# Optimization experiments

Hardware: AMD Instinct MI355X
Metric: run time of the kernel (lower is better)

The kernel has to match this reference:

```python
import jax, jax.numpy as jnp
import numpy as np

EPS = 1e-6

def _ste(x, xq):
    return x + jax.lax.stop_gradient(xq - x)

def rmsnorm(x, w):
    return x * jax.lax.rsqrt(jnp.mean(x * x, axis=-1, keepdims=True) + EPS) * w

def act_quant(x):
    # per-token absmax int8 quantization (BitNet b1.58)
    s = 127.0 / jnp.clip(jnp.max(jnp.abs(x), axis=-1, keepdims=True), 1e-5)
    return _ste(x, jnp.clip(jnp.round(x * s), -128, 127) / s)

def w_quant(w):
    # per-tensor mean-absmax ternary quantization
    s = 1.0 / jnp.clip(jnp.mean(jnp.abs(w)), 1e-5)
    return _ste(w, jnp.clip(jnp.round(w * s), -1, 1) / s)

def bitlinear(x, w):
    return act_quant(x) @ w_quant(w).T

def snake_beta(x, log_a, log_b):
    a = jnp.exp(log_a)
    b = jnp.exp(log_b)
    s = jnp.sin(a * x)
    return x + (1.0 / (b + 1e-9)) * s * s

def ffn(x, nw, w1, la, lb, w2):
    h = bitlinear(rmsnorm(x, nw), w1)
    return bitlinear(snake_beta(h, la, lb), w2)

def mha(x, nw, ipw, ipb, opw, opb, num_heads):
    B, T, D = x.shape
    hd = D // num_heads
    xn = rmsnorm(x, nw)
    qkv = xn @ ipw.T + ipb  # [B,T,3D]
    q, k, v = jnp.split(qkv, 3, axis=-1)
    def heads(t):
        return t.reshape(B, T, num_heads, hd).transpose(0, 2, 1, 3)  # [B,H,T,hd]
    q, k, v = heads(q), heads(k), heads(v)
    scores = jnp.einsum('bhqd,bhkd->bhqk', q, k) / jnp.sqrt(jnp.asarray(hd, x.dtype))
    attn = jax.nn.softmax(scores, axis=-1)
    o = jnp.einsum('bhqk,bhkd->bhqd', attn, v)
    o = o.transpose(0, 2, 1, 3).reshape(B, T, D)
    return o @ opw.T + opb

def conv_branch(x, nw, pw1, dw, dwb, bg, bb, bm, bv, la, lb, pw2, K):
    B, T, D = x.shape
    h = rmsnorm(x, nw)
    h = bitlinear(h, pw1)  # [B,T,2D] (1x1 BitConv1d)
    a, g = jnp.split(h, 2, axis=-1)
    h = a * jax.nn.sigmoid(g)  # GLU over channels
    hc = h.transpose(0, 2, 1)  # [B,D,T]
    hc = jax.lax.conv_general_dilated(
        hc, dw, window_strides=(1,), padding=[(K // 2, K // 2)],
        feature_group_count=D, dimension_numbers=('NCH', 'OIH', 'NCH'))
    hc = hc + dwb[None, :, None]
    hc = (hc - bm[None, :, None]) * jax.lax.rsqrt(bv[None, :, None] + 1e-5) * bg[None, :, None] + bb[None, :, None]
    h = hc.transpose(0, 2, 1)  # [B,T,D]
    h = snake_beta(h, la, lb)
    return bitlinear(h, pw2)

def setup_inputs() -> dict:
    key = jax.random.key(0)
    B, T, D, H, K = 4, 2048, 512, 8, 31
    ks = jax.random.split(key, 16)
    n = lambda k, s: (jax.random.normal(k, s, jnp.float32) * 0.02)
    d = {
        'x': jax.random.normal(ks[0], (B, T, D), jnp.float32),
        'ff1_norm_w': jnp.ones((D,), jnp.float32),
        'ff1_w1': n(ks[1], (4 * D, D)), 'ff1_a': jnp.zeros((4 * D,), jnp.float32),
        'ff1_b': jnp.zeros((4 * D,), jnp.float32), 'ff1_w2': n(ks[2], (D, 4 * D)),
        'attn_norm_w': jnp.ones((D,), jnp.float32),
        'in_proj_w': n(ks[3], (3 * D, D)), 'in_proj_b': jnp.zeros((3 * D,), jnp.float32),
        'out_proj_w': n(ks[4], (D, D)), 'out_proj_b': jnp.zeros((D,), jnp.float32),
        'conv_norm_w': jnp.ones((D,), jnp.float32),
        'pw1_w': n(ks[5], (2 * D, D)),
        'dw_w': n(ks[6], (D, 1, K)), 'dw_b': jnp.zeros((D,), jnp.float32),
        'bn_g': jnp.ones((D,), jnp.float32), 'bn_b': jnp.zeros((D,), jnp.float32),
        'bn_m': jnp.zeros((D,), jnp.float32), 'bn_v': jnp.ones((D,), jnp.float32),
        'snake_a': jnp.zeros((D,), jnp.float32), 'snake_b': jnp.zeros((D,), jnp.float32),
        'pw2_w': n(ks[7], (D, D)),
        'ff2_norm_w': jnp.ones((D,), jnp.float32),
        'ff2_w1': n(ks[8], (4 * D, D)), 'ff2_a': jnp.zeros((4 * D,), jnp.float32),
        'ff2_b': jnp.zeros((4 * D,), jnp.float32), 'ff2_w2': n(ks[9], (D, 4 * D)),
        'final_norm_w': jnp.ones((D,), jnp.float32),
    }
    return d

def reference(x, ff1_norm_w, ff1_w1, ff1_a, ff1_b, ff1_w2, attn_norm_w, in_proj_w, in_proj_b, out_proj_w, out_proj_b, conv_norm_w, pw1_w, dw_w, dw_b, bn_g, bn_b, bn_m, bn_v, snake_a, snake_b, pw2_w, ff2_norm_w, ff2_w1, ff2_a, ff2_b, ff2_w2, final_norm_w):
    H, K = 8, 31
    x = x + 0.5 * ffn(x, ff1_norm_w, ff1_w1, ff1_a, ff1_b, ff1_w2)
    x = x + mha(x, attn_norm_w, in_proj_w, in_proj_b, out_proj_w, out_proj_b, H)
    x = x + conv_branch(x, conv_norm_w, pw1_w, dw_w, dw_b, bn_g, bn_b, bn_m, bn_v, snake_a, snake_b, pw2_w, K)
    x = x + 0.5 * ffn(x, ff2_norm_w, ff2_w1, ff2_a, ff2_b, ff2_w2)
    return rmsnorm(x, final_norm_w)
```

## Files before the change

### kernel.cpp

```cpp
#include <hip/hip_runtime.h>
#include <math.h>


typedef int   v4i __attribute__((ext_vector_type(4)));
typedef float v4f __attribute__((ext_vector_type(4)));
typedef float v16f __attribute__((ext_vector_type(16)));
typedef short v8s __attribute__((ext_vector_type(8)));
typedef unsigned short u16;

#define GLOAD_LDS(g, l) __builtin_amdgcn_global_load_lds( \
    (const __attribute__((address_space(1))) void*)(g),   \
    (__attribute__((address_space(3))) void*)(l), 16, 0, 0)

__device__ __forceinline__ float blk_sum256(float v, float* sm) {
#pragma unroll
  for (int m = 32; m; m >>= 1) v += __shfl_xor(v, m);
  int w = threadIdx.x >> 6;
  __syncthreads();
  if ((threadIdx.x & 63) == 0) sm[w] = v;
  __syncthreads();
  return sm[0] + sm[1] + sm[2] + sm[3];
}

__device__ __forceinline__ u16 f2bf(float f) {
  union { float f; unsigned u; } x;
  x.f = f;
  unsigned r = x.u + 0x7fffu + ((x.u >> 16) & 1u);
  return (u16)(r >> 16);
}

__device__ __forceinline__ float bf2f(u16 u) {
  union { unsigned u; float f; } x;
  x.u = ((unsigned)u) << 16;
  return x.f;
}

__device__ __forceinline__ void xcd_tiles(int& tx, int& ty) {
  int nx = gridDim.x;
  int flat = blockIdx.y * nx + blockIdx.x;
  int nwg = nx * gridDim.y;
  int cpx = nwg >> 3;
  int swz = (flat & 7) * cpx + (flat >> 3);
  ty = swz / nx;
  tx = swz - ty * nx;
}

__global__ __launch_bounds__(256) void wabs_stage1(
    const float* __restrict__ w0, const float* __restrict__ w1,
    const float* __restrict__ w2, const float* __restrict__ w3,
    const float* __restrict__ w4, const float* __restrict__ w5,
    float* __restrict__ part) {
  __shared__ float sm[4];
  const float* ws[6] = {w0, w1, w2, w3, w4, w5};
  const int ns[6] = {1048576, 1048576, 524288, 262144, 1048576, 1048576};
  int widx = blockIdx.x >> 6;
  int chunk = blockIdx.x & 63;
  const float* w = ws[widx];
  int n = ns[widx];
  float s = 0.f;
  for (int i = chunk * 256 + threadIdx.x; i < n; i += 64 * 256) s += fabsf(w[i]);
  s = blk_sum256(s, sm);
  if (threadIdx.x == 0) part[widx * 64 + chunk] = s;
}

__global__ __launch_bounds__(256) void wquant_all(
    const float* __restrict__ w0, const float* __restrict__ w1,
    const float* __restrict__ w2, const float* __restrict__ w3,
    const float* __restrict__ w4, const float* __restrict__ w5,
    const float* __restrict__ part, float* __restrict__ scales,
    signed char* __restrict__ out) {
  const float* ws[6] = {w0, w1, w2, w3, w4, w5};
  const int ns[6] = {1048576, 1048576, 524288, 262144, 1048576, 1048576};
  const int offs[6] = {0, 1048576, 2097152, 2621440, 2883584, 3932160};
  int widx = blockIdx.y;
  const float* w = ws[widx];
  int n = ns[widx];
  signed char* o = out + offs[widx];
  float ssum = 0.f;
#pragma unroll 8
  for (int i = 0; i < 64; ++i) ssum += part[widx * 64 + i];
  float wsc = fmaxf(ssum / (float)n, 1e-5f);
  if (blockIdx.x == 0 && threadIdx.x == 0) scales[widx] = wsc;
  float s = 1.0f / wsc;
  for (int i = blockIdx.x * 256 + threadIdx.x; i < n; i += 128 * 256)
    o[i] = (signed char)(int)fminf(fmaxf(rintf(w[i] * s), -1.f), 1.f);
}

__global__ __launch_bounds__(256) void wcvt_tabs(
    const float* __restrict__ ip, const float* __restrict__ op, u16* __restrict__ wb,
    const float* __restrict__ a1, const float* __restrict__ b1,
    const float* __restrict__ a2, const float* __restrict__ b2,
    float* __restrict__ tabs) {
  int bid = blockIdx.x;
  if (bid < 1024) {
    int i = bid * 256 + threadIdx.x;
    float4 f;
    if (i < 196608) f = *(const float4*)(ip + (size_t)i * 4);
    else f = *(const float4*)(op + (size_t)(i - 196608) * 4);
    u16* dst = wb + (size_t)i * 4;
    dst[0] = f2bf(f.x); dst[1] = f2bf(f.y); dst[2] = f2bf(f.z); dst[3] = f2bf(f.w);
  } else {
    int i = (bid - 1024) * 256 + threadIdx.x;
    if (i < 2048) {
      tabs[i] = __expf(a1[i]);
      tabs[2048 + i] = 1.0f / (__expf(b1[i]) + 1e-9f);
      tabs[4096 + i] = __expf(a2[i]);
      tabs[6144 + i] = 1.0f / (__expf(b2[i]) + 1e-9f);
    }
  }
}

__global__ __launch_bounds__(256) void rmsnorm_f32x(
    const float* __restrict__ x, const float* __restrict__ w,
    signed char* __restrict__ out8, u16* __restrict__ xbf,
    float* __restrict__ dq) {
  const int tid = threadIdx.x;
  const int lane = tid & 63, wv = tid >> 6;
  const int row = blockIdx.x * 4 + wv;
  const int c0 = lane * 8;
  const float* xr = x + (size_t)row * 512 + c0;
  float4 f0 = *(const float4*)xr;
  float4 f1 = *(const float4*)(xr + 4);
  float fin[8] = {f0.x, f0.y, f0.z, f0.w, f1.x, f1.y, f1.z, f1.w};
  v8s xb;
  float v[8];
  float ss = 0.f;
#pragma unroll
  for (int j = 0; j < 8; ++j) {
    u16 b = f2bf(fin[j]);
    xb[j] = (short)b;
    v[j] = bf2f(b);
    ss = fmaf(v[j], v[j], ss);
  }
  *(v8s*)(xbf + (size_t)row * 512 + c0) = xb;
#pragma unroll
  for (int m = 1; m < 64; m <<= 1) ss += __shfl_xor(ss, m);
  float sc = 1.0f / sqrtf(ss * (1.0f / 512.0f) + 1e-6f);
  float4 w0 = *(const float4*)(w + c0);
  float4 w1 = *(const float4*)(w + c0 + 4);
  float wv8[8] = {w0.x, w0.y, w0.z, w0.w, w1.x, w1.y, w1.z, w1.w};
  float y[8];
  float am = 0.f;
#pragma unroll
  for (int j = 0; j < 8; ++j) {
    y[j] = v[j] * sc * wv8[j];
    am = fmaxf(am, fabsf(y[j]));
  }
#pragma unroll
  for (int m = 1; m < 64; m <<= 1) am = fmaxf(am, __shfl_xor(am, m));
  float amc = fmaxf(am, 1e-5f);
  float s = 127.0f / amc;
  unsigned long long pkt = 0;
#pragma unroll
  for (int j = 0; j < 8; ++j) {
    int q = (int)rintf(y[j] * s);
    pkt |= ((unsigned long long)(unsigned char)(signed char)q) << (8 * j);
  }
  *(unsigned long long*)(out8 + (size_t)row * 512 + c0) = pkt;
  if (lane == 0) dq[row] = amc * (1.0f / 127.0f);
}

__global__ __launch_bounds__(256) void rmsnorm_wave(
    const u16* __restrict__ x, const float* __restrict__ w, int mode,
    float* __restrict__ outf, signed char* __restrict__ out8,
    u16* __restrict__ outb, float* __restrict__ dq) {
  const int tid = threadIdx.x;
  const int lane = tid & 63, wv = tid >> 6;
  const int row = blockIdx.x * 4 + wv;
  const int c0 = lane * 8;
  v8s xv = *(const v8s*)(x + (size_t)row * 512 + c0);
  float v[8];
  float ss = 0.f;
#pragma unroll
  for (int j = 0; j < 8; ++j) {
    v[j] = bf2f((u16)xv[j]);
    ss = fmaf(v[j], v[j], ss);
  }
#pragma unroll
  for (int m = 1; m < 64; m <<= 1) ss += __shfl_xor(ss, m);
  float sc = 1.0f / sqrtf(ss * (1.0f / 512.0f) + 1e-6f);
  float4 w0 = *(const float4*)(w + c0);
  float4 w1 = *(const float4*)(w + c0 + 4);
  float wv8[8] = {w0.x, w0.y, w0.z, w0.w, w1.x, w1.y, w1.z, w1.w};
  float y[8];
#pragma unroll
  for (int j = 0; j < 8; ++j) y[j] = v[j] * sc * wv8[j];
  if (mode == 0) {
    float* o = outf + (size_t)row * 512 + c0;
    *(float4*)o = make_float4(y[0], y[1], y[2], y[3]);
    *(float4*)(o + 4) = make_float4(y[4], y[5], y[6], y[7]);
  } else if (mode == 1) {
    float am = 0.f;
#pragma unroll
    for (int j = 0; j < 8; ++j) am = fmaxf(am, fabsf(y[j]));
#pragma unroll
    for (int m = 1; m < 64; m <<= 1) am = fmaxf(am, __shfl_xor(am, m));
    float amc = fmaxf(am, 1e-5f);
    float s = 127.0f / amc;
    unsigned long long pkt = 0;
#pragma unroll
    for (int j = 0; j < 8; ++j) {
      int q = (int)rintf(y[j] * s);
      pkt |= ((unsigned long long)(unsigned char)(signed char)q) << (8 * j);
    }
    *(unsigned long long*)(out8 + (size_t)row * 512 + c0) = pkt;
    if (lane == 0) dq[row] = amc * (1.0f / 127.0f);
  } else {
    v8s o;
#pragma unroll
    for (int j = 0; j < 8; ++j) o[j] = (short)f2bf(y[j]);
    *(v8s*)(outb + (size_t)row * 512 + c0) = o;
  }
}

__global__ __launch_bounds__(256) void snake_wave(
    const u16* __restrict__ h, const float* __restrict__ ta, const float* __restrict__ tb,
    signed char* __restrict__ out, float* __restrict__ dq) {
  const int tid = threadIdx.x;
  const int lane = tid & 63, wv = tid >> 6;
  const int row = blockIdx.x * 4 + wv;
  const u16* hr = h + (size_t)row * 2048;
  float vals[32];
  float am = 0.f;
#pragma unroll
  for (int g = 0; g < 4; ++g) {
    int c0 = g * 512 + lane * 8;
    v8s hv = *(const v8s*)(hr + c0);
    float4 ta0 = *(const float4*)(ta + c0);
    float4 ta1 = *(const float4*)(ta + c0 + 4);
    float4 tb0 = *(const float4*)(tb + c0);
    float4 tb1 = *(const float4*)(tb + c0 + 4);
    float sa[8] = {ta0.x, ta0.y, ta0.z, ta0.w, ta1.x, ta1.y, ta1.z, ta1.w};
    float sib[8] = {tb0.x, tb0.y, tb0.z, tb0.w, tb1.x, tb1.y, tb1.z, tb1.w};
#pragma unroll
    for (int j = 0; j < 8; ++j) {
      float v = bf2f((u16)hv[j]);
      float s = __sinf(sa[j] * v);
      v += s * s * sib[j];
      vals[g * 8 + j] = v;
      am = fmaxf(am, fabsf(v));
    }
  }
#pragma unroll
  for (int m = 1; m < 64; m <<= 1) am = fmaxf(am, __shfl_xor(am, m));
  float amc = fmaxf(am, 1e-5f);
  float s = 127.0f / amc;
#pragma unroll
  for (int g = 0; g < 4; ++g) {
    unsigned long long pkt = 0;
#pragma unroll
    for (int j = 0; j < 8; ++j) {
      int q = (int)rintf(vals[g * 8 + j] * s);
      pkt |= ((unsigned long long)(unsigned char)(signed char)q) << (8 * j);
    }
    *(unsigned long long*)(out + (size_t)row * 2048 + g * 512 + lane * 8) = pkt;
  }
  if (lane == 0) dq[row] = amc * (1.0f / 127.0f);
}

__global__ __launch_bounds__(256) void rowquant_wave(
    const u16* __restrict__ in, signed char* __restrict__ out, float* __restrict__ dq) {
  const int tid = threadIdx.x;
  const int lane = tid & 63, wv = tid >> 6;
  const int row = blockIdx.x * 4 + wv;
  const int c0 = lane * 8;
  v8s xv = *(const v8s*)(in + (size_t)row * 512 + c0);
  float v[8];
  float am = 0.f;
#pragma unroll
  for (int j = 0; j < 8; ++j) {
    v[j] = bf2f((u16)xv[j]);
    am = fmaxf(am, fabsf(v[j]));
  }
#pragma unroll
  for (int m = 1; m < 64; m <<= 1) am = fmaxf(am, __shfl_xor(am, m));
  float amc = fmaxf(am, 1e-5f);
  float s = 127.0f / amc;
  unsigned long long pkt = 0;
#pragma unroll
  for (int j = 0; j < 8; ++j) {
    int q = (int)rintf(v[j] * s);
    pkt |= ((unsigned long long)(unsigned char)(signed char)q) << (8 * j);
  }
  *(unsigned long long*)(out + (size_t)row * 512 + c0) = pkt;
  if (lane == 0) dq[row] = amc * (1.0f / 127.0f);
}

template <int BN, int OM>
__global__ __launch_bounds__(256) void gemm_i8_t(
    const signed char* __restrict__ A, const signed char* __restrict__ B,
    const float* __restrict__ wsp, const float* __restrict__ adq,
    const u16* __restrict__ resid, float rscale,
    u16* __restrict__ outb, int N, int K) {
  constexpr int JF = BN / 32;
  __shared__ signed char As[16384];
  __shared__ signed char Bs[BN * 128];
  const int tid = threadIdx.x;
  int txc, tyc;
  xcd_tiles(txc, tyc);
  const int m0 = tyc << 7;
  const int n0 = txc * BN;
  const int lane = tid & 63;
  const int wv = tid >> 6;
  const int wr = (wv >> 1) << 6, wc = (wv & 1) * (16 * JF);
  const int r15 = lane & 15, khi = lane >> 4;
  const int srow = tid >> 3;
  const int sslot = (tid & 7) ^ (srow & 7);
  const signed char* Ag = A + (size_t)(m0 + srow) * K + sslot * 16;
  const signed char* Bg = B + (size_t)(n0 + srow) * K + sslot * 16;
  const size_t row32 = (size_t)32 * K;

  int aoff[4][2], boff[JF][2];
#pragma unroll
  for (int i = 0; i < 4; ++i) {
    int r = wr + i * 16 + r15;
#pragma unroll
    for (int s = 0; s < 2; ++s)
      aoff[i][s] = r * 128 + (((s << 2) + khi) ^ (r & 7)) * 16;
  }
#pragma unroll
  for (int j = 0; j < JF; ++j) {
    int c = wc + j * 16 + r15;
#pragma unroll
    for (int s = 0; s < 2; ++s)
      boff[j][s] = c * 128 + (((s << 2) + khi) ^ (c & 7)) * 16;
  }
  v4i acc[4][JF] = {};
  for (int k0 = 0; k0 < K; k0 += 128) {
    __syncthreads();
#pragma unroll
    for (int c = 0; c < 4; ++c)
      GLOAD_LDS(Ag + c * row32 + k0, As + c * 4096 + tid * 16);
#pragma unroll
    for (int c = 0; c < BN / 32; ++c)
      GLOAD_LDS(Bg + c * row32 + k0, Bs + c * 4096 + tid * 16);
    __syncthreads();
    v4i a[4][2], b[JF][2];
#pragma unroll
    for (int i = 0; i < 4; ++i) {
      a[i][0] = *(const v4i*)(As + aoff[i][0]);
      a[i][1] = *(const v4i*)(As + aoff[i][1]);
    }
#pragma unroll
    for (int j = 0; j < JF; ++j) {
      b[j][0] = *(const v4i*)(Bs + boff[j][0]);
      b[j][1] = *(const v4i*)(Bs + boff[j][1]);
    }
#pragma unroll
    for (int i = 0; i < 4; ++i)
#pragma unroll
      for (int j = 0; j < JF; ++j) {
        acc[i][j] = __builtin_amdgcn_mfma_i32_16x16x64_i8(a[i][0], b[j][0], acc[i][j], 0, 0, 0);
        acc[i][j] = __builtin_amdgcn_mfma_i32_16x16x64_i8(a[i][1], b[j][1], acc[i][j], 0, 0, 0);
      }
  }
  const float wsc = *wsp;
#pragma unroll
  for (int i = 0; i < 4; ++i) {
    int rb = m0 + wr + i * 16 + (khi << 2);
    float dqv[4];
#pragma unroll
    for (int rr = 0; rr < 4; ++rr) dqv[rr] = adq[rb + rr] * wsc;
#pragma unroll
    for (int j = 0; j < JF; ++j) {
      int col = n0 + wc + j * 16 + r15;
#pragma unroll
      for (int rr = 0; rr < 4; ++rr) {
        size_t idx = (size_t)(rb + rr) * N + col;
        float v = (float)acc[i][j][rr] * dqv[rr];
        if constexpr (OM == 0) outb[idx] = f2bf(v);
        else outb[idx] = f2bf(fmaf(rscale, v, bf2f(resid[idx])));
      }
    }
  }
}

template <int BN, int OM>
__global__ __launch_bounds__(256) void gemm_bf16_t(
    const u16* __restrict__ A, const u16* __restrict__ B,
    const float* __restrict__ bias, const u16* __restrict__ resid,
    u16* __restrict__ outb, int N, int K) {
  constexpr int JF = BN / 32;
  __shared__ signed char As[8192];
  __shared__ signed char Bs[BN * 64];
  const int tid = threadIdx.x;
  int txc, tyc;
  xcd_tiles(txc, tyc);
  const int m0 = tyc << 7;
  const int n0 = txc * BN;
  const int lane = tid & 63;
  const int wv = tid >> 6;
  const int wr = (wv >> 1) << 6, wc = (wv & 1) * (16 * JF);
  const int r15 = lane & 15, khi = lane >> 4;
  const int srow = tid >> 2;
  const int sslot = (tid & 3) ^ ((srow >> 1) & 3);
  const int K2 = K * 2;
  const signed char* Ag = (const signed char*)A + (size_t)(m0 + srow) * K2 + sslot * 16;
  const signed char* Bg = (const signed char*)B + (size_t)(n0 + srow) * K2 + sslot * 16;
  const size_t half = (size_t)64 * K2;

  int aoff[4], boff[JF];
#pragma unroll
  for (int i = 0; i < 4; ++i) {
    int r = wr + i * 16 + r15;
    aoff[i] = r * 64 + ((khi ^ ((r >> 1) & 3)) << 4);
  }
#pragma unroll
  for (int j = 0; j < JF; ++j) {
    int c = wc + j * 16 + r15;
    boff[j] = c * 64 + ((khi ^ ((c >> 1) & 3)) << 4);
  }
  v4f acc[4][JF] = {};
  for (int kb = 0; kb < K2; kb += 64) {
    __syncthreads();
    GLOAD_LDS(Ag + kb, As + tid * 16);
    GLOAD_LDS(Ag + half + kb, As + 4096 + tid * 16);
    GLOAD_LDS(Bg + kb, Bs + tid * 16);
    if constexpr (BN == 128) GLOAD_LDS(Bg + half + kb, Bs + 4096 + tid * 16);
    __syncthreads();
    v8s a[4], b[JF];
#pragma unroll
    for (int i = 0; i < 4; ++i) a[i] = *(const v8s*)(As + aoff[i]);
#pragma unroll
    for (int j = 0; j < JF; ++j) b[j] = *(const v8s*)(Bs + boff[j]);
#pragma unroll
    for (int i = 0; i < 4; ++i)
#pragma unroll
      for (int j = 0; j < JF; ++j)
        acc[i][j] = __builtin_amdgcn_mfma_f32_16x16x32_bf16(a[i], b[j], acc[i][j], 0, 0, 0);
  }
#pragma unroll
  for (int i = 0; i < 4; ++i) {
    int rb = m0 + wr + i * 16 + (khi << 2);
#pragma unroll
    for (int j = 0; j < JF; ++j) {
      int col = n0 + wc + j * 16 + r15;
      float bv = bias[col];
#pragma unroll
      for (int rr = 0; rr < 4; ++rr) {
        float v = acc[i][j][rr] + bv;
        if constexpr (OM == 2) {
          int rowb = rb + rr;
          int tin = rowb & 31;
          int seg = col >> 9;
          int cc = col & 511;
          int h2 = cc >> 6, d = cc & 63;
          size_t base = ((size_t)(((rowb >> 11) * 8 + h2) * 64 + ((rowb & 2047) >> 5))) * 6144;
          size_t off;
          if (seg == 0)
            off = (size_t)(8 + (d >> 4)) * 512 + ((((d >> 3) & 1) << 5) + tin) * 8 + (d & 7);
          else if (seg == 1)
            off = (size_t)(d >> 4) * 512 + ((((d >> 3) & 1) << 5) + tin) * 8 + (d & 7);
          else
            off = (size_t)(4 + ((d >> 5) << 1) + (tin >> 4)) * 512 +
                  ((((tin >> 3) & 1) << 5) + (d & 31)) * 8 + (tin & 7);
          outb[base + off] = f2bf(v);
        } else {
          size_t idx = (size_t)(rb + rr) * N + col;
          if constexpr (OM == 0) outb[idx] = f2bf(v);
          else outb[idx] = f2bf(bf2f(resid[idx]) + v);
        }
      }
    }
  }
}

__global__ __launch_bounds__(256) void attn32(
    const u16* __restrict__ kvqp, u16* __restrict__ opart, float* __restrict__ ml) {
  __shared__ u16 KV[2][4096];
  const int tid = threadIdx.x;
  const int lane = tid & 63;
  const int wv = tid >> 6;
  const int l31 = lane & 31;
  const int hi = lane >> 5;
  const int bh = blockIdx.y;
  const int z = blockIdx.z;
  const int b = bh >> 3, h = bh & 7;
  const int qt = blockIdx.x * 4 + wv;
  const int q0 = qt << 5;
  const float C = 0.18033688011112042f;

  v8s qf[4];
  {
    const u16* qb = kvqp + ((size_t)(bh * 64 + qt)) * 6144 + lane * 8;
#pragma unroll
    for (int ks = 0; ks < 4; ++ks) qf[ks] = *(const v8s*)(qb + (8 + ks) * 512);
  }
  v16f o0 = {}, o1 = {};
  float l_run = 0.f;

  const u16* tb = kvqp + ((size_t)(bh * 64 + z * 32)) * 6144;

  GLOAD_LDS(tb + tid * 8, &KV[0][tid * 8]);
  GLOAD_LDS(tb + 2048 + tid * 8, &KV[0][2048 + tid * 8]);
  __syncthreads();

  int cur = 0;
  for (int t = 0; t < 32; ++t) {
    if (t < 31) {
      const u16* nb = tb + (size_t)(t + 1) * 6144;
      GLOAD_LDS(nb + tid * 8, &KV[cur ^ 1][tid * 8]);
      GLOAD_LDS(nb + 2048 + tid * 8, &KV[cur ^ 1][2048 + tid * 8]);
    }
    v8s kf[4], vf[4];
#pragma unroll
    for (int ks = 0; ks < 4; ++ks) kf[ks] = *(const v8s*)(&KV[cur][ks * 512 + lane * 8]);
#pragma unroll
    for (int j = 0; j < 4; ++j) vf[j] = *(const v8s*)(&KV[cur][2048 + j * 512 + lane * 8]);

    __builtin_amdgcn_s_setprio(1);
    v16f sacc = {};
#pragma unroll
    for (int ks = 0; ks < 4; ++ks)
      sacc = __builtin_amdgcn_mfma_f32_32x32x16_bf16(kf[ks], qf[ks], sacc, 0, 0, 0);
    __builtin_amdgcn_s_setprio(0);

    float s[16];
#pragma unroll
    for (int r = 0; r < 16; ++r) s[r] = exp2f(sacc[r] * C);

    {
      float a0 = (s[0] + s[1]) + (s[2] + s[3]);
      float a1 = (s[4] + s[5]) + (s[6] + s[7]);
      float a2 = (s[8] + s[9]) + (s[10] + s[11]);
      float a3 = (s[12] + s[13]) + (s[14] + s[15]);
      float ls = (a0 + a1) + (a2 + a3);
      float tsw = ls;
      asm("v_permlane32_swap_b32 %0, %1" : "+v"(tsw), "+v"(ls));
      l_run += ls + tsw;
    }

    unsigned pk[8];
#pragma unroll
    for (int g = 0; g < 8; ++g) {
      unsigned u;
      asm("v_cvt_pk_bf16_f32 %0, %1, %2" : "=v"(u) : "v"(s[2 * g]), "v"(s[2 * g + 1]));
      pk[g] = u;
    }
    asm("v_permlane32_swap_b32 %0, %1" : "+v"(pk[2]), "+v"(pk[0]));
    asm("v_permlane32_swap_b32 %0, %1" : "+v"(pk[3]), "+v"(pk[1]));
    asm("v_permlane32_swap_b32 %0, %1" : "+v"(pk[6]), "+v"(pk[4]));
    asm("v_permlane32_swap_b32 %0, %1" : "+v"(pk[7]), "+v"(pk[5]));
    v4i w0, w1;
    w0[0] = pk[0]; w0[1] = pk[1]; w0[2] = pk[2]; w0[3] = pk[3];
    w1[0] = pk[4]; w1[1] = pk[5]; w1[2] = pk[6]; w1[3] = pk[7];
    v8s pf0 = *(v8s*)&w0;
    v8s pf1 = *(v8s*)&w1;

    __builtin_amdgcn_s_setprio(1);
    o0 = __builtin_amdgcn_mfma_f32_32x32x16_bf16(vf[0], pf0, o0, 0, 0, 0);
    o0 = __builtin_amdgcn_mfma_f32_32x32x16_bf16(vf[1], pf1, o0, 0, 0, 0);
    o1 = __builtin_amdgcn_mfma_f32_32x32x16_bf16(vf[2], pf0, o1, 0, 0, 0);
    o1 = __builtin_amdgcn_mfma_f32_32x32x16_bf16(vf[3], pf1, o1, 0, 0, 0);
    __builtin_amdgcn_s_setprio(0);

    __syncthreads();
    cur ^= 1;
  }

  float inv = 1.0f / l_run;
  u16* orow = opart + (size_t)z * 4194304 + (size_t)(b * 2048 + q0 + l31) * 512 + h * 64;
#pragma unroll
  for (int dt = 0; dt < 2; ++dt) {
#pragma unroll
    for (int g = 0; g < 8; ++g) {
      int d = dt * 32 + ((2 * g) & 3) + 8 * (g >> 1) + 4 * hi;
      float a = (dt ? o1[2 * g] : o0[2 * g]) * inv;
      float bv = (dt ? o1[2 * g + 1] : o0[2 * g + 1]) * inv;
      unsigned u;
      asm("v_cvt_pk_bf16_f32 %0, %1, %2" : "=v"(u) : "v"(a), "v"(bv));
      *(unsigned*)(orow + d) = u;
    }
  }
  if (hi == 0) {
    size_t mi = (size_t)(z * 8192 + b * 2048 + q0 + l31) * 8 + h;
    ml[mi] = l_run;
  }
}

__global__ __launch_bounds__(256) void attn_merge(
    const u16* __restrict__ opart, const float* __restrict__ ml,
    u16* __restrict__ attno) {
  __shared__ float wsm[2][8];
  const int r = blockIdx.x, tid = threadIdx.x;
  if (tid < 8) {
    float l0 = ml[(size_t)r * 8 + tid];
    float l1 = ml[(size_t)(8192 + r) * 8 + tid];
    float inv = 1.0f / (l0 + l1);
    wsm[0][tid] = l0 * inv;
    wsm[1][tid] = l1 * inv;
  }
  __syncthreads();
  int c = tid * 2;
  int hh = c >> 6;
  float x0 = 0.f, x1 = 0.f;
#pragma unroll
  for (int z = 0; z < 2; ++z) {
    unsigned p = *(const unsigned*)(opart + (size_t)z * 4194304 + (size_t)r * 512 + c);
    float w = wsm[z][hh];
    x0 = fmaf(bf2f((u16)p), w, x0);
    x1 = fmaf(bf2f((u16)(p >> 16)), w, x1);
  }
  unsigned u;
  asm("v_cvt_pk_bf16_f32 %0, %1, %2" : "=v"(u) : "v"(x0), "v"(x1));
  *(unsigned*)(attno + (size_t)r * 512 + c) = u;
}

__global__ __launch_bounds__(256) void dwconv_fused(
    const u16* __restrict__ g3, const float* __restrict__ dww,
    const float* __restrict__ dwb, const float* __restrict__ bng,
    const float* __restrict__ bnb, const float* __restrict__ bnm,
    const float* __restrict__ bnv, const float* __restrict__ la,
    const float* __restrict__ lb, u16* __restrict__ outp) {
  __shared__ float IN[160 * 64];
  __shared__ float WT[1984];
  __shared__ float PRM[4][64];
  const int tid = threadIdx.x;
  const int cg = blockIdx.x << 6;
  const int t0 = blockIdx.y << 7;
  const int bb = blockIdx.z;

  if (tid < 64) {
    int c = cg + tid;
    float sc = bng[c] / sqrtf(bnv[c] + 1e-5f);
    PRM[0][tid] = sc;
    PRM[1][tid] = (dwb[c] - bnm[c]) * sc + bnb[c];
    PRM[2][tid] = __expf(la[c]);
    PRM[3][tid] = 1.0f / (__expf(lb[c]) + 1e-9f);
  }
  for (int i = tid; i < 1984; i += 256) WT[i] = dww[cg * 31 + i];

#pragma unroll
  for (int p = 0; p < 5; ++p) {
    int r = p * 32 + (tid >> 3);
    int t = t0 - 16 + r;
    int c8 = (tid & 7) << 3;
    float4 lo = make_float4(0.f, 0.f, 0.f, 0.f);
    float4 hv = make_float4(0.f, 0.f, 0.f, 0.f);
    if (t >= 0 && t < 2048) {
      const u16* rp = g3 + ((size_t)(bb * 2048 + t)) * 1024 + cg + c8;
      v8s a8 = *(const v8s*)rp;
      v8s g8 = *(const v8s*)(rp + 512);
      float va[8];
#pragma unroll
      for (int j = 0; j < 8; ++j) {
        float fa = bf2f((u16)a8[j]);
        float fg = bf2f((u16)g8[j]);
        va[j] = fa / (1.f + __expf(-fg));
      }
      lo = make_float4(va[0], va[1], va[2], va[3]);
      hv = make_float4(va[4], va[5], va[6], va[7]);
    }
    *(float4*)&IN[r * 64 + c8] = lo;
    *(float4*)&IN[r * 64 + c8 + 4] = hv;
  }
  __syncthreads();

  const int ch = tid & 63;
  const int tg = tid >> 6;
  const float sc = PRM[0][ch], sh = PRM[1][ch], sa = PRM[2][ch], sib = PRM[3][ch];
  float w[31];
#pragma unroll
  for (int k = 0; k < 31; ++k) w[k] = WT[ch * 31 + k];

  for (int pass = 0; pass < 4; ++pass) {
    int tl = pass * 32 + tg * 8;
    float x[38];
#pragma unroll
    for (int i = 0; i < 38; ++i) x[i] = IN[(tl + 1 + i) * 64 + ch];
    float acc[8] = {0.f, 0.f, 0.f, 0.f, 0.f, 0.f, 0.f, 0.f};
#pragma unroll
    for (int k = 0; k < 31; ++k)
#pragma unroll
      for (int j = 0; j < 8; ++j) acc[j] = fmaf(x[k + j], w[k], acc[j]);
#pragma unroll
    for (int j = 0; j < 8; ++j) {
      float v = acc[j] * sc + sh;
      float s = __sinf(sa * v);
      v += s * s * sib;
      outp[((size_t)(bb * 2048 + t0 + tl + j)) * 512 + cg + ch] = f2bf(v);
    }
  }
}

extern "C" void kernel_launch(void* const* d_in, const int* in_sizes, int n_in,
                              void* d_out, int out_size, void* d_ws, size_t ws_size,
                              hipStream_t stream) {
  const float* x_in = (const float*)d_in[0];
  const float* ff1_norm_w = (const float*)d_in[1];
  const float* ff1_w1 = (const float*)d_in[2];
  const float* ff1_a = (const float*)d_in[3];
  const float* ff1_b = (const float*)d_in[4];
  const float* ff1_w2 = (const float*)d_in[5];
  const float* attn_norm_w = (const float*)d_in[6];
  const float* in_proj_w = (const float*)d_in[7];
  const float* in_proj_b = (const float*)d_in[8];
  const float* out_proj_w = (const float*)d_in[9];
  const float* out_proj_b = (const float*)d_in[10];
  const float* conv_norm_w = (const float*)d_in[11];
  const float* pw1_w = (const float*)d_in[12];
  const float* dw_w = (const float*)d_in[13];
  const float* dw_b = (const float*)d_in[14];
  const float* bn_g = (const float*)d_in[15];
  const float* bn_b = (const float*)d_in[16];
  const float* bn_m = (const float*)d_in[17];
  const float* bn_v = (const float*)d_in[18];
  const float* snake_a = (const float*)d_in[19];
  const float* snake_b = (const float*)d_in[20];
  const float* pw2_w = (const float*)d_in[21];
  const float* ff2_norm_w = (const float*)d_in[22];
  const float* ff2_w1 = (const float*)d_in[23];
  const float* ff2_a = (const float*)d_in[24];
  const float* ff2_b = (const float*)d_in[25];
  const float* ff2_w2 = (const float*)d_in[26];
  const float* final_norm_w = (const float*)d_in[27];
  float* out = (float*)d_out;

  char* ws = (char*)d_ws;
  u16* x_bf = (u16*)(ws + 0);
  u16* x_cur = (u16*)(ws + 8388608);
  u16* kvqp = (u16*)(ws + 41943040);
  u16* opart = (u16*)(ws + 67108864);
  u16* attno = (u16*)(ws + 100663296);
  float* ml = (float*)(ws + 109051904);
  u16* h_b = (u16*)(ws + 16777216);
  u16* g3b = (u16*)(ws + 16777216);
  u16* convout = (u16*)(ws + 50331648);
  signed char* a8a = (signed char*)(ws + 83886080);
  signed char* a8b = (signed char*)(ws + 88080384);
  u16* xnb = (u16*)(ws + 104857600);
  signed char* wq = (signed char*)(ws + 113246208);
  signed char* wq_w1 = wq;
  signed char* wq_w2 = wq + 1048576;
  signed char* wq_p1 = wq + 2097152;
  signed char* wq_p2 = wq + 2621440;
  signed char* wq_f21 = wq + 2883584;
  signed char* wq_f22 = wq + 3932160;
  u16* wb = (u16*)(ws + 118226944);
  u16* wb_ip = wb;
  u16* wb_op = wb + 786432;
  float* scales = (float*)(ws + 120324096);
  float* partials = (float*)(ws + 120324352);
  float* ascale = (float*)(ws + 120325888);
  float* tabs = (float*)(ws + 120358912);

  wabs_stage1<<<384, 256, 0, stream>>>(ff1_w1, ff1_w2, pw1_w, pw2_w, ff2_w1, ff2_w2, partials);
  wquant_all<<<dim3(128, 6), 256, 0, stream>>>(ff1_w1, ff1_w2, pw1_w, pw2_w, ff2_w1, ff2_w2,
                                               partials, scales, wq);
  wcvt_tabs<<<1032, 256, 0, stream>>>(in_proj_w, out_proj_w, wb, ff1_a, ff1_b, ff2_a, ff2_b,
                                      tabs);

  rmsnorm_f32x<<<2048, 256, 0, stream>>>(x_in, ff1_norm_w, a8a, x_bf, ascale);
  gemm_i8_t<128, 0><<<dim3(16, 64), 256, 0, stream>>>(
      a8a, wq_w1, scales + 0, ascale, nullptr, 1.0f, h_b, 2048, 512);
  snake_wave<<<2048, 256, 0, stream>>>(h_b, tabs, tabs + 2048, a8b, ascale);
  gemm_i8_t<64, 1><<<dim3(8, 64), 256, 0, stream>>>(
      a8b, wq_w2, scales + 1, ascale, x_bf, 0.5f, x_cur, 512, 2048);

  rmsnorm_wave<<<2048, 256, 0, stream>>>(x_cur, attn_norm_w, 2, nullptr, nullptr, xnb, nullptr);
  gemm_bf16_t<128, 2><<<dim3(12, 64), 256, 0, stream>>>(
      xnb, wb_ip, in_proj_b, nullptr, kvqp, 1536, 512);
  attn32<<<dim3(16, 32, 2), 256, 0, stream>>>(kvqp, opart, ml);
  attn_merge<<<8192, 256, 0, stream>>>(opart, ml, attno);
  gemm_bf16_t<64, 1><<<dim3(8, 64), 256, 0, stream>>>(
      attno, wb_op, out_proj_b, x_cur, x_cur, 512, 512);

  rmsnorm_wave<<<2048, 256, 0, stream>>>(x_cur, conv_norm_w, 1, nullptr, a8a, nullptr, ascale);
  gemm_i8_t<128, 0><<<dim3(8, 64), 256, 0, stream>>>(
      a8a, wq_p1, scales + 2, ascale, nullptr, 1.0f, g3b, 1024, 512);
  dwconv_fused<<<dim3(8, 16, 4), 256, 0, stream>>>(g3b, dw_w, dw_b, bn_g, bn_b, bn_m, bn_v,
                                                   snake_a, snake_b, convout);
  rowquant_wave<<<2048, 256, 0, stream>>>(convout, a8a, ascale);
  gemm_i8_t<64, 1><<<dim3(8, 64), 256, 0, stream>>>(
      a8a, wq_p2, scales + 3, ascale, x_cur, 1.0f, x_cur, 512, 512);

  rmsnorm_wave<<<2048, 256, 0, stream>>>(x_cur, ff2_norm_w, 1, nullptr, a8a, nullptr, ascale);
  gemm_i8_t<128, 0><<<dim3(16, 64), 256, 0, stream>>>(
      a8a, wq_f21, scales + 4, ascale, nullptr, 1.0f, h_b, 2048, 512);
  snake_wave<<<2048, 256, 0, stream>>>(h_b, tabs + 4096, tabs + 6144, a8b, ascale);
  gemm_i8_t<64, 1><<<dim3(8, 64), 256, 0, stream>>>(
      a8b, wq_f22, scales + 5, ascale, x_cur, 0.5f, x_cur, 512, 2048);

  rmsnorm_wave<<<2048, 256, 0, stream>>>(x_cur, final_norm_w, 0, out, nullptr, nullptr, nullptr);
}
```

Baseline: 297.9 us.

## Fuse snake activation into FFN1 GEMM epilogue and drop attention split-K merge

The snake-beta activation moves into the epilogue of the first FFN int8 GEMM, using a new OM==2 mode, so the following row-quant kernel only computes absmax and quantizes. Separately, attention no longer splits the key range in two along blockIdx.z. Each block now loops over all 64 key tiles and writes the normalized output directly, which removes the partial-output buffer writes and the attn_merge kernel. In exchange the attention grid is halved, so there is less parallelism and a longer serial loop per block. The sin in the epilogue also adds some work to the GEMM.

```diff
diff --git a/kernel.cpp b/kernel.cpp
--- a/kernel.cpp
+++ b/kernel.cpp
@@ -213,9 +213,8 @@
   }
 }
 
-__global__ __launch_bounds__(256) void snake_wave(
-    const u16* __restrict__ h, const float* __restrict__ ta, const float* __restrict__ tb,
-    signed char* __restrict__ out, float* __restrict__ dq) {
+__global__ __launch_bounds__(256) void rq2048_wave(
+    const u16* __restrict__ h, signed char* __restrict__ out, float* __restrict__ dq) {
   const int tid = threadIdx.x;
   const int lane = tid & 63, wv = tid >> 6;
   const int row = blockIdx.x * 4 + wv;
@@ -226,17 +225,9 @@
   for (int g = 0; g < 4; ++g) {
     int c0 = g * 512 + lane * 8;
     v8s hv = *(const v8s*)(hr + c0);
-    float4 ta0 = *(const float4*)(ta + c0);
-    float4 ta1 = *(const float4*)(ta + c0 + 4);
-    float4 tb0 = *(const float4*)(tb + c0);
-    float4 tb1 = *(const float4*)(tb + c0 + 4);
-    float sa[8] = {ta0.x, ta0.y, ta0.z, ta0.w, ta1.x, ta1.y, ta1.z, ta1.w};
-    float sib[8] = {tb0.x, tb0.y, tb0.z, tb0.w, tb1.x, tb1.y, tb1.z, tb1.w};
 #pragma unroll
     for (int j = 0; j < 8; ++j) {
       float v = bf2f((u16)hv[j]);
-      float s = __sinf(sa[j] * v);
-      v += s * s * sib[j];
       vals[g * 8 + j] = v;
       am = fmaxf(am, fabsf(v));
     }
@@ -291,7 +282,8 @@
     const signed char* __restrict__ A, const signed char* __restrict__ B,
     const float* __restrict__ wsp, const float* __restrict__ adq,
     const u16* __restrict__ resid, float rscale,
-    u16* __restrict__ outb, int N, int K) {
+    u16* __restrict__ outb, int N, int K,
+    const float* __restrict__ ta, const float* __restrict__ tb) {
   constexpr int JF = BN / 32;
   __shared__ signed char As[16384];
   __shared__ signed char Bs[BN * 128];
@@ -364,12 +356,20 @@
 #pragma unroll
     for (int j = 0; j < JF; ++j) {
       int col = n0 + wc + j * 16 + r15;
+      float sa, sib;
+      if constexpr (OM == 2) { sa = ta[col]; sib = tb[col]; }
 #pragma unroll
       for (int rr = 0; rr < 4; ++rr) {
         size_t idx = (size_t)(rb + rr) * N + col;
         float v = (float)acc[i][j][rr] * dqv[rr];
-        if constexpr (OM == 0) outb[idx] = f2bf(v);
-        else outb[idx] = f2bf(fmaf(rscale, v, bf2f(resid[idx])));
+        if constexpr (OM == 0) {
+          outb[idx] = f2bf(v);
+        } else if constexpr (OM == 1) {
+          outb[idx] = f2bf(fmaf(rscale, v, bf2f(resid[idx])));
+        } else {
+          float sn = __sinf(sa * v);
+          outb[idx] = f2bf(v + sn * sn * sib);
+        }
       }
     }
   }
@@ -466,7 +466,7 @@
 }
 
 __global__ __launch_bounds__(256) void attn32(
-    const u16* __restrict__ kvqp, u16* __restrict__ opart, float* __restrict__ ml) {
+    const u16* __restrict__ kvqp, u16* __restrict__ attno) {
   __shared__ u16 KV[2][4096];
   const int tid = threadIdx.x;
   const int lane = tid & 63;
@@ -474,7 +474,6 @@
   const int l31 = lane & 31;
   const int hi = lane >> 5;
   const int bh = blockIdx.y;
-  const int z = blockIdx.z;
   const int b = bh >> 3, h = bh & 7;
   const int qt = blockIdx.x * 4 + wv;
   const int q0 = qt << 5;
@@ -489,15 +488,15 @@
   v16f o0 = {}, o1 = {};
   float l_run = 0.f;
 
-  const u16* tb = kvqp + ((size_t)(bh * 64 + z * 32)) * 6144;
+  const u16* tb = kvqp + ((size_t)(bh * 64)) * 6144;
 
   GLOAD_LDS(tb + tid * 8, &KV[0][tid * 8]);
   GLOAD_LDS(tb + 2048 + tid * 8, &KV[0][2048 + tid * 8]);
   __syncthreads();
 
   int cur = 0;
-  for (int t = 0; t < 32; ++t) {
-    if (t < 31) {
+  for (int t = 0; t < 64; ++t) {
+    if (t < 63) {
       const u16* nb = tb + (size_t)(t + 1) * 6144;
       GLOAD_LDS(nb + tid * 8, &KV[cur ^ 1][tid * 8]);
       GLOAD_LDS(nb + 2048 + tid * 8, &KV[cur ^ 1][2048 + tid * 8]);
@@ -559,7 +558,7 @@
   }
 
   float inv = 1.0f / l_run;
-  u16* orow = opart + (size_t)z * 4194304 + (size_t)(b * 2048 + q0 + l31) * 512 + h * 64;
+  u16* orow = attno + (size_t)(b * 2048 + q0 + l31) * 512 + h * 64;
 #pragma unroll
   for (int dt = 0; dt < 2; ++dt) {
 #pragma unroll
@@ -572,38 +571,6 @@
       *(unsigned*)(orow + d) = u;
     }
   }
-  if (hi == 0) {
-    size_t mi = (size_t)(z * 8192 + b * 2048 + q0 + l31) * 8 + h;
-    ml[mi] = l_run;
-  }
-}
-
-__global__ __launch_bounds__(256) void attn_merge(
-    const u16* __restrict__ opart, const float* __restrict__ ml,
-    u16* __restrict__ attno) {
-  __shared__ float wsm[2][8];
-  const int r = blockIdx.x, tid = threadIdx.x;
-  if (tid < 8) {
-    float l0 = ml[(size_t)r * 8 + tid];
-    float l1 = ml[(size_t)(8192 + r) * 8 + tid];
-    float inv = 1.0f / (l0 + l1);
-    wsm[0][tid] = l0 * inv;
-    wsm[1][tid] = l1 * inv;
-  }
-  __syncthreads();
-  int c = tid * 2;
-  int hh = c >> 6;
-  float x0 = 0.f, x1 = 0.f;
-#pragma unroll
-  for (int z = 0; z < 2; ++z) {
-    unsigned p = *(const unsigned*)(opart + (size_t)z * 4194304 + (size_t)r * 512 + c);
-    float w = wsm[z][hh];
-    x0 = fmaf(bf2f((u16)p), w, x0);
-    x1 = fmaf(bf2f((u16)(p >> 16)), w, x1);
-  }
-  unsigned u;
-  asm("v_cvt_pk_bf16_f32 %0, %1, %2" : "=v"(u) : "v"(x0), "v"(x1));
-  *(unsigned*)(attno + (size_t)r * 512 + c) = u;
 }
 
 __global__ __launch_bounds__(256) void dwconv_fused(
@@ -720,9 +687,7 @@
   u16* x_bf = (u16*)(ws + 0);
   u16* x_cur = (u16*)(ws + 8388608);
   u16* kvqp = (u16*)(ws + 41943040);
-  u16* opart = (u16*)(ws + 67108864);
   u16* attno = (u16*)(ws + 100663296);
-  float* ml = (float*)(ws + 109051904);
   u16* h_b = (u16*)(ws + 16777216);
   u16* g3b = (u16*)(ws + 16777216);
   u16* convout = (u16*)(ws + 50331648);
@@ -751,35 +716,34 @@
                                       tabs);
 
   rmsnorm_f32x<<<2048, 256, 0, stream>>>(x_in, ff1_norm_w, a8a, x_bf, ascale);
-  gemm_i8_t<128, 0><<<dim3(16, 64), 256, 0, stream>>>(
-      a8a, wq_w1, scales + 0, ascale, nullptr, 1.0f, h_b, 2048, 512);
-  snake_wave<<<2048, 256, 0, stream>>>(h_b, tabs, tabs + 2048, a8b, ascale);
+  gemm_i8_t<128, 2><<<dim3(16, 64), 256, 0, stream>>>(
+      a8a, wq_w1, scales + 0, ascale, nullptr, 1.0f, h_b, 2048, 512, tabs, tabs + 2048);
+  rq2048_wave<<<2048, 256, 0, stream>>>(h_b, a8b, ascale);
   gemm_i8_t<64, 1><<<dim3(8, 64), 256, 0, stream>>>(
-      a8b, wq_w2, scales + 1, ascale, x_bf, 0.5f, x_cur, 512, 2048);
+      a8b, wq_w2, scales + 1, ascale, x_bf, 0.5f, x_cur, 512, 2048, nullptr, nullptr);
 
   rmsnorm_wave<<<2048, 256, 0, stream>>>(x_cur, attn_norm_w, 2, nullptr, nullptr, xnb, nullptr);
   gemm_bf16_t<128, 2><<<dim3(12, 64), 256, 0, stream>>>(
       xnb, wb_ip, in_proj_b, nullptr, kvqp, 1536, 512);
-  attn32<<<dim3(16, 32, 2), 256, 0, stream>>>(kvqp, opart, ml);
-  attn_merge<<<8192, 256, 0, stream>>>(opart, ml, attno);
+  attn32<<<dim3(16, 32), 256, 0, stream>>>(kvqp, attno);
   gemm_bf16_t<64, 1><<<dim3(8, 64), 256, 0, stream>>>(
       attno, wb_op, out_proj_b, x_cur, x_cur, 512, 512);
 
   rmsnorm_wave<<<2048, 256, 0, stream>>>(x_cur, conv_norm_w, 1, nullptr, a8a, nullptr, ascale);
   gemm_i8_t<128, 0><<<dim3(8, 64), 256, 0, stream>>>(
-      a8a, wq_p1, scales + 2, ascale, nullptr, 1.0f, g3b, 1024, 512);
+      a8a, wq_p1, scales + 2, ascale, nullptr, 1.0f, g3b, 1024, 512, nullptr, nullptr);
   dwconv_fused<<<dim3(8, 16, 4), 256, 0, stream>>>(g3b, dw_w, dw_b, bn_g, bn_b, bn_m, bn_v,
                                                    snake_a, snake_b, convout);
   rowquant_wave<<<2048, 256, 0, stream>>>(convout, a8a, ascale);
   gemm_i8_t<64, 1><<<dim3(8, 64), 256, 0, stream>>>(
-      a8a, wq_p2, scales + 3, ascale, x_cur, 1.0f, x_cur, 512, 512);
+      a8a, wq_p2, scales + 3, ascale, x_cur, 1.0f, x_cur, 512, 512, nullptr, nullptr);
 
   rmsnorm_wave<<<2048, 256, 0, stream>>>(x_cur, ff2_norm_w, 1, nullptr, a8a, nullptr, ascale);
-  gemm_i8_t<128, 0><<<dim3(16, 64), 256, 0, stream>>>(
-      a8a, wq_f21, scales + 4, ascale, nullptr, 1.0f, h_b, 2048, 512);
-  snake_wave<<<2048, 256, 0, stream>>>(h_b, tabs + 4096, tabs + 6144, a8b, ascale);
+  gemm_i8_t<128, 2><<<dim3(16, 64), 256, 0, stream>>>(
+      a8a, wq_f21, scales + 4, ascale, nullptr, 1.0f, h_b, 2048, 512, tabs + 4096, tabs + 6144);
+  rq2048_wave<<<2048, 256, 0, stream>>>(h_b, a8b, ascale);
   gemm_i8_t<64, 1><<<dim3(8, 64), 256, 0, stream>>>(
-      a8b, wq_f22, scales + 5, ascale, x_cur, 0.5f, x_cur, 512, 2048);
+      a8b, wq_f22, scales + 5, ascale, x_cur, 0.5f, x_cur, 512, 2048, nullptr, nullptr);
 
   rmsnorm_wave<<<2048, 256, 0, stream>>>(x_cur, final_norm_w, 0, out, nullptr, nullptr, nullptr);
 }
```

Result: no change. 292.4 us (-1.9%).
